# Optimization experiments

Measured on AMD Instinct MI355X. Metric: run time of the kernel, lower is better.

The kernel has to match this reference:

```python
import jax, jax.numpy as jnp
import numpy as np


def setup_inputs() -> dict:
    key = jax.random.key(0)
    ks = jax.random.split(key, 8)
    C = 256
    Cq = C // 8  # 32
    B, H, W = 4, 64, 64
    x = jax.random.normal(ks[0], (B, C, H, W), dtype=jnp.float32)
    wq = jax.random.normal(ks[1], (Cq, C), dtype=jnp.float32) * (1.0 / np.sqrt(C))
    bq = jax.random.normal(ks[2], (Cq,), dtype=jnp.float32) * 0.01
    wk = jax.random.normal(ks[3], (Cq, C), dtype=jnp.float32) * (1.0 / np.sqrt(C))
    bk = jax.random.normal(ks[4], (Cq,), dtype=jnp.float32) * 0.01
    wv = jax.random.normal(ks[5], (C, C), dtype=jnp.float32) * (1.0 / np.sqrt(C))
    bv = jax.random.normal(ks[6], (C,), dtype=jnp.float32) * 0.01
    gamma = jax.random.normal(ks[7], (1,), dtype=jnp.float32)
    return {"x": x, "wq": wq, "bq": bq, "wk": wk, "bk": bk,
            "wv": wv, "bv": bv, "gamma": gamma}


def reference(x, wq, bq, wk, bk, wv, bv, gamma):
    B, C, H, W = x.shape
    N = H * W
    xf = x.reshape(B, C, N)  # [B, C, N] flattened spatial
    # 1x1 convs == per-position linear projections
    q = jnp.einsum('oc,bcn->bno', wq, xf) + bq          # [B, N, Cq]
    k = jnp.einsum('oc,bcn->bon', wk, xf) + bk[:, None]  # [B, Cq, N]
    v = jnp.einsum('oc,bcn->bon', wv, xf) + bv[:, None]  # [B, C, N]
    attn = jax.nn.softmax(jnp.einsum('bnc,bcm->bnm', q, k), axis=-1)  # [B, N, N]
    # out[b,c,n] = sum_m v[b,c,m] * attn[n,m]
    out = jnp.einsum('bcm,bnm->bcn', v, attn).reshape(B, C, H, W)
    return gamma[0] * out + x
```

## Files before the change

kernel.cpp:

```cpp
#include <hip/hip_runtime.h>

#define BB 4
#define CC 256
#define CQ 32
#define NN 4096

#define QT_OFF 0
#define KT_OFF (BB*NN*CQ)
#define VT_OFF (2*BB*NN*CQ)
#define WB_OFF (VT_OFF + BB*CC*NN)
#define BIAS_OFF (WB_OFF + 320*256)

#define LDS_BARRIER() asm volatile("s_waitcnt lgkmcnt(0)\ns_barrier" ::: "memory")

typedef __attribute__((ext_vector_type(8))) short bf16x8;
typedef __attribute__((ext_vector_type(4))) short bf16x4;
typedef __attribute__((ext_vector_type(4))) float f32x4;

__device__ inline unsigned short f2bf(float f) {
    unsigned int u = __float_as_uint(f);
    u += 0x7fffu + ((u >> 16) & 1u);
    return (unsigned short)(u >> 16);
}

__global__ __launch_bounds__(256) void prepw_kernel(
    const float* __restrict__ wq, const float* __restrict__ bq,
    const float* __restrict__ wk, const float* __restrict__ bk,
    const float* __restrict__ wv, const float* __restrict__ bv,
    unsigned short* __restrict__ ws)
{
    unsigned short* Wb = ws + WB_OFF;
    float* Bias = (float*)(ws + BIAS_OFF);
    int idx = blockIdx.x * 256 + threadIdx.x;
    if (idx < 320 * 256) {
        int row = idx >> 8, col = idx & 255;
        float v = row < 32 ? wq[row * 256 + col]
                : row < 64 ? wk[(row - 32) * 256 + col]
                           : wv[(row - 64) * 256 + col];
        Wb[idx] = f2bf(v);
    }
    if (idx < 320)
        Bias[idx] = idx < 32 ? bq[idx] : idx < 64 ? bk[idx - 32] : bv[idx - 64];
}

__global__ __launch_bounds__(256, 2) void qkv_kernel(
    const float* __restrict__ x, unsigned short* __restrict__ ws)
{
    __shared__ __align__(16) unsigned short xs[32][264];
    __shared__ __align__(16) unsigned short vs[256][40];
    const int t = threadIdx.x;
    const int w = t >> 6, l = t & 63, quad = l >> 4, lc = l & 15;
    const int b = blockIdx.y, n0 = blockIdx.x * 32;

    unsigned short* qT = ws + QT_OFF;
    unsigned short* kT = ws + KT_OFF;
    const unsigned short* Wb = ws + WB_OFF;
    const float* Bias = (const float*)(ws + BIAS_OFF);

    const float* xb = x + (size_t)(b * CC) * NN + n0;
    {
        const int nq = t & 7, swz = (nq & 3) << 3;
#pragma unroll
        for (int u = 0; u < 2; ++u) {
            const int c0 = (t >> 3) * 4 + u * 128;
            f32x4 r0 = *(const f32x4*)&xb[(size_t)(c0 + 0) * NN + nq * 4];
            f32x4 r1 = *(const f32x4*)&xb[(size_t)(c0 + 1) * NN + nq * 4];
            f32x4 r2 = *(const f32x4*)&xb[(size_t)(c0 + 2) * NN + nq * 4];
            f32x4 r3 = *(const f32x4*)&xb[(size_t)(c0 + 3) * NN + nq * 4];
            const int cs = c0 ^ swz;
#pragma unroll
            for (int k = 0; k < 4; ++k) {
                bf16x4 w4;
                w4[0] = (short)f2bf(r0[k]);
                w4[1] = (short)f2bf(r1[k]);
                w4[2] = (short)f2bf(r2[k]);
                w4[3] = (short)f2bf(r3[k]);
                *(bf16x4*)&xs[nq * 4 + k][cs] = w4;
            }
        }
    }
    __syncthreads();

    f32x4 acc[5][2];
#pragma unroll
    for (int j = 0; j < 5; ++j) {
        f32x4 b4 = *(const f32x4*)&Bias[(w * 5 + j) * 16 + quad * 4];
        acc[j][0] = b4; acc[j][1] = b4;
    }

#pragma unroll
    for (int s = 0; s < 8; ++s) {
        bf16x8 Af[5], Bf[2];
#pragma unroll
        for (int j = 0; j < 5; ++j)
            Af[j] = *(const bf16x8*)&Wb[((w * 5 + j) * 16 + lc) * 256 + s * 32 + quad * 8];
#pragma unroll
        for (int nt = 0; nt < 2; ++nt) {
            int pos = nt * 16 + lc;
            int col = (s * 32 + quad * 8) ^ (((pos >> 2) & 3) << 3);
            Bf[nt] = *(const bf16x8*)&xs[pos][col];
        }
#pragma unroll
        for (int j = 0; j < 5; ++j)
#pragma unroll
            for (int nt = 0; nt < 2; ++nt)
                acc[j][nt] = __builtin_amdgcn_mfma_f32_16x16x32_bf16(Af[j], Bf[nt], acc[j][nt], 0, 0, 0);
    }

#pragma unroll
    for (int j = 0; j < 5; ++j) {
        int ot = w * 5 + j;
#pragma unroll
        for (int nt = 0; nt < 2; ++nt) {
            if (ot < 4) {
                bf16x4 pk;
#pragma unroll
                for (int i = 0; i < 4; ++i) pk[i] = (short)f2bf(acc[j][nt][i]);
                unsigned short* bas = (ot < 2 ? qT : kT);
                int ocl = (ot & 1) * 16 + quad * 4;
                *(bf16x4*)&bas[((size_t)(b * NN + n0 + nt * 16 + lc)) * CQ + ocl] = pk;
            } else {
#pragma unroll
                for (int i = 0; i < 4; ++i)
                    vs[(ot - 4) * 16 + quad * 4 + i][nt * 16 + lc] = f2bf(acc[j][nt][i]);
            }
        }
    }
    __syncthreads();

    const int mt = n0 >> 6, hb = (n0 >> 5) & 1;
    unsigned short* vt = ws + VT_OFF + ((size_t)(b * 64 + mt) * 16) * 1024 + hb * 512;
#pragma unroll
    for (int p = 0; p < 4; ++p) {
        int ci = p * 256 + t;
        int ct = ci >> 6, g = (ci >> 4) & 3, lcp = ci & 15;
        bf16x8 chunk = *(const bf16x8*)&vs[ct * 16 + lcp][g * 8];
        *(bf16x8*)&vt[(size_t)ct * 1024 + g * 128 + lcp * 8] = chunk;
    }
}

__global__ __launch_bounds__(512, 2) void attn_kernel(
    const float* __restrict__ x, const unsigned short* __restrict__ ws,
    const float* __restrict__ gamma, float* __restrict__ out)
{
    __shared__ __align__(16) unsigned short Ps[2][4][4][512];
    __shared__ __align__(16) float lSpart[2][64];

    const int t = threadIdx.x;
    const int w = t >> 6, l = t & 63, quad = l >> 4, lc = l & 15;
    const int id = blockIdx.x, xcd = id & 7;
    const int b = xcd >> 1;
    const int n0 = (((id >> 3) << 1) | (xcd & 1)) * 64;

    const int qg = w & 3;
    const int kh = w >> 2;
    const int cb = w * 32;

    const unsigned short* qT = ws + QT_OFF;
    const unsigned short* kb = ws + KT_OFF + (size_t)b * NN * CQ;
    const unsigned short* vb = ws + VT_OFF + ((size_t)b << 20);

    const bf16x8 bqf =
        *(const bf16x8*)&qT[((size_t)(b * NN + n0 + qg * 16 + lc)) * CQ + quad * 8];

    bf16x8 kA[4], kB[4];
    auto loadK = [&](bf16x8* kr, int tt) {
        int m0 = (tt & 31) * 128 + kh * 64;
#pragma unroll
        for (int j = 0; j < 4; ++j)
            kr[j] = *(const bf16x8*)&kb[(size_t)(m0 + j * 16 + lc) * CQ + quad * 8];
    };

    bf16x8 vA[2][4], vB[2][4];
    auto loadV = [&](bf16x8 (*vr)[4], int tt) {
#pragma unroll
        for (int c = 0; c < 2; ++c) {
            int ct = w * 2 + c;
#pragma unroll
            for (int k4 = 0; k4 < 4; ++k4) {
                int m = (tt & 31) * 2 + (k4 >> 1);
                vr[c][k4] = *(const bf16x8*)&vb[((size_t)m * 16 + ct) * 1024 + (k4 & 1) * 512 + l * 8];
            }
        }
    };

    f32x4 acc[4][2];
#pragma unroll
    for (int i = 0; i < 4; ++i)
#pragma unroll
        for (int j = 0; j < 2; ++j) acc[i][j] = (f32x4){0.f, 0.f, 0.f, 0.f};
    f32x4 sn[4];
    float lacc = 0.f;
    const f32x4 z = {0.f, 0.f, 0.f, 0.f};

    auto expj = [&](int pp, int j) {
        bf16x4 pk;
#pragma unroll
        for (int i = 0; i < 4; ++i) {
            float p = __expf(sn[j][i]);
            lacc += p;
            pk[i] = (short)f2bf(p);
        }
        int ks = kh * 2 + (j >> 1);
        int lanep = ((2 * j + (quad >> 1)) & 3) * 16 + lc;
        *(bf16x4*)&Ps[pp][qg][ks][lanep * 8 + (quad & 1) * 4] = pk;
    };

    auto pvks = [&](int ks, bf16x8 (*vr)[4], const bf16x8* ap) {
        __builtin_amdgcn_s_setprio(1);
#pragma unroll
        for (int qs = 0; qs < 4; ++qs)
#pragma unroll
            for (int c = 0; c < 2; ++c)
                acc[qs][c] = __builtin_amdgcn_mfma_f32_16x16x32_bf16(ap[qs], vr[c][ks], acc[qs][c], 0, 0, 0);
        __builtin_amdgcn_s_setprio(0);
    };

    auto body = [&](int tt, int pp, bf16x8* kUse, bf16x8* kNext,
                    bf16x8 (*vUse)[4], bf16x8 (*vNext)[4]) {
        loadV(vNext, tt + 1);
#pragma unroll
        for (int j = 0; j < 4; ++j)
            sn[j] = __builtin_amdgcn_mfma_f32_16x16x32_bf16(kUse[j], bqf, z, 0, 0, 0);
        loadK(kNext, tt + 2);
#pragma unroll
        for (int ks = 0; ks < 4; ++ks) {
            bf16x8 ap[4];
#pragma unroll
            for (int qs = 0; qs < 4; ++qs)
                ap[qs] = *(const bf16x8*)&Ps[pp][qs][ks][l * 8];
            expj(pp ^ 1, ks);
            pvks(ks, vUse, ap);
        }
        LDS_BARRIER();
    };

    loadK(kA, 0);
#pragma unroll
    for (int j = 0; j < 4; ++j)
        sn[j] = __builtin_amdgcn_mfma_f32_16x16x32_bf16(kA[j], bqf, z, 0, 0, 0);
    loadK(kA, 1);
#pragma unroll
    for (int j = 0; j < 4; ++j) expj(0, j);
    loadV(vA, 0);
    LDS_BARRIER();

    for (int it = 0; it < 15; ++it) {
        body(2 * it,     0, kA, kB, vA, vB);
        body(2 * it + 1, 1, kB, kA, vB, vA);
    }
    body(30, 0, kA, kB, vA, vB);
#pragma unroll
    for (int ks = 0; ks < 4; ++ks) {
        bf16x8 ap[4];
#pragma unroll
        for (int qs = 0; qs < 4; ++qs)
            ap[qs] = *(const bf16x8*)&Ps[1][qs][ks][l * 8];
        pvks(ks, vB, ap);
    }

    lacc += __shfl_xor(lacc, 16);
    lacc += __shfl_xor(lacc, 32);
    if (quad == 0) lSpart[kh][qg * 16 + lc] = lacc;
    LDS_BARRIER();

    const float g = gamma[0];
#pragma unroll
    for (int qs = 0; qs < 4; ++qs) {
        f32x4 l0 = *(const f32x4*)&lSpart[0][qs * 16 + quad * 4];
        f32x4 l1 = *(const f32x4*)&lSpart[1][qs * 16 + quad * 4];
        f32x4 rl;
#pragma unroll
        for (int i = 0; i < 4; ++i) rl[i] = 1.f / (l0[i] + l1[i]);
#pragma unroll
        for (int c2 = 0; c2 < 2; ++c2) {
            int c = cb + c2 * 16 + lc;
            size_t base = ((size_t)(b * CC + c)) * NN + n0 + qs * 16 + quad * 4;
            f32x4 xr = *(const f32x4*)&x[base];
            f32x4 o;
#pragma unroll
            for (int i = 0; i < 4; ++i) o[i] = g * acc[qs][c2][i] * rl[i] + xr[i];
            *(f32x4*)&out[base] = o;
        }
    }
}

extern "C" void kernel_launch(void* const* d_in, const int* in_sizes, int n_in,
                              void* d_out, int out_size, void* d_ws, size_t ws_size,
                              hipStream_t stream) {
    const float* x     = (const float*)d_in[0];
    const float* wq    = (const float*)d_in[1];
    const float* bq    = (const float*)d_in[2];
    const float* wk    = (const float*)d_in[3];
    const float* bk    = (const float*)d_in[4];
    const float* wv    = (const float*)d_in[5];
    const float* bv    = (const float*)d_in[6];
    const float* gamma = (const float*)d_in[7];
    float* out = (float*)d_out;
    unsigned short* ws = (unsigned short*)d_ws;

    prepw_kernel<<<320, 256, 0, stream>>>(wq, bq, wk, bk, wv, bv, ws);
    dim3 g1(NN / 32, BB);
    qkv_kernel<<<g1, 256, 0, stream>>>(x, ws);
    attn_kernel<<<256, 512, 0, stream>>>(x, ws, gamma, out);
}
```

Measured before the change: 145.0 us.

## Specialize warps into QK/softmax producers and PV consumers

```diff
diff --git a/kernel.cpp b/kernel.cpp
--- a/kernel.cpp
+++ b/kernel.cpp
@@ -144,143 +144,157 @@
     const float* __restrict__ gamma, float* __restrict__ out)
 {
     __shared__ __align__(16) unsigned short Ps[2][4][4][512];
-    __shared__ __align__(16) float lSpart[2][64];
+    __shared__ __align__(16) float lS[64];
 
     const int t = threadIdx.x;
     const int w = t >> 6, l = t & 63, quad = l >> 4, lc = l & 15;
     const int id = blockIdx.x, xcd = id & 7;
     const int b = xcd >> 1;
     const int n0 = (((id >> 3) << 1) | (xcd & 1)) * 64;
-
-    const int qg = w & 3;
-    const int kh = w >> 2;
-    const int cb = w * 32;
+    const int r = w >> 1;
 
     const unsigned short* qT = ws + QT_OFF;
     const unsigned short* kb = ws + KT_OFF + (size_t)b * NN * CQ;
     const unsigned short* vb = ws + VT_OFF + ((size_t)b << 20);
 
-    const bf16x8 bqf =
-        *(const bf16x8*)&qT[((size_t)(b * NN + n0 + qg * 16 + lc)) * CQ + quad * 8];
-
-    bf16x8 kA[4], kB[4];
-    auto loadK = [&](bf16x8* kr, int tt) {
-        int m0 = (tt & 31) * 128 + kh * 64;
-#pragma unroll
-        for (int j = 0; j < 4; ++j)
-            kr[j] = *(const bf16x8*)&kb[(size_t)(m0 + j * 16 + lc) * CQ + quad * 8];
-    };
-
-    bf16x8 vA[2][4], vB[2][4];
-    auto loadV = [&](bf16x8 (*vr)[4], int tt) {
-#pragma unroll
-        for (int c = 0; c < 2; ++c) {
-            int ct = w * 2 + c;
-#pragma unroll
-            for (int k4 = 0; k4 < 4; ++k4) {
-                int m = (tt & 31) * 2 + (k4 >> 1);
-                vr[c][k4] = *(const bf16x8*)&vb[((size_t)m * 16 + ct) * 1024 + (k4 & 1) * 512 + l * 8];
-            }
-        }
-    };
-
-    f32x4 acc[4][2];
-#pragma unroll
-    for (int i = 0; i < 4; ++i)
-#pragma unroll
-        for (int j = 0; j < 2; ++j) acc[i][j] = (f32x4){0.f, 0.f, 0.f, 0.f};
-    f32x4 sn[4];
-    float lacc = 0.f;
-    const f32x4 z = {0.f, 0.f, 0.f, 0.f};
-
-    auto expj = [&](int pp, int j) {
-        bf16x4 pk;
-#pragma unroll
-        for (int i = 0; i < 4; ++i) {
-            float p = __expf(sn[j][i]);
-            lacc += p;
-            pk[i] = (short)f2bf(p);
-        }
-        int ks = kh * 2 + (j >> 1);
-        int lanep = ((2 * j + (quad >> 1)) & 3) * 16 + lc;
-        *(bf16x4*)&Ps[pp][qg][ks][lanep * 8 + (quad & 1) * 4] = pk;
-    };
-
-    auto pvks = [&](int ks, bf16x8 (*vr)[4], const bf16x8* ap) {
-        __builtin_amdgcn_s_setprio(1);
-#pragma unroll
-        for (int qs = 0; qs < 4; ++qs)
-#pragma unroll
-            for (int c = 0; c < 2; ++c)
-                acc[qs][c] = __builtin_amdgcn_mfma_f32_16x16x32_bf16(ap[qs], vr[c][ks], acc[qs][c], 0, 0, 0);
-        __builtin_amdgcn_s_setprio(0);
-    };
-
-    auto body = [&](int tt, int pp, bf16x8* kUse, bf16x8* kNext,
-                    bf16x8 (*vUse)[4], bf16x8 (*vNext)[4]) {
-        loadV(vNext, tt + 1);
-#pragma unroll
-        for (int j = 0; j < 4; ++j)
-            sn[j] = __builtin_amdgcn_mfma_f32_16x16x32_bf16(kUse[j], bqf, z, 0, 0, 0);
-        loadK(kNext, tt + 2);
-#pragma unroll
-        for (int ks = 0; ks < 4; ++ks) {
+    if ((w & 1) == 0) {
+        const int qg = r;
+        const bf16x8 bqf =
+            *(const bf16x8*)&qT[((size_t)(b * NN + n0 + qg * 16 + lc)) * CQ + quad * 8];
+        const f32x4 z = {0.f, 0.f, 0.f, 0.f};
+
+        bf16x8 kA[8], kB[8];
+        auto loadK = [&](bf16x8* kr, int tt) {
+            int m0 = (tt & 31) * 128;
+#pragma unroll
+            for (int j = 0; j < 8; ++j)
+                kr[j] = *(const bf16x8*)&kb[(size_t)(m0 + j * 16 + lc) * CQ + quad * 8];
+        };
+
+        f32x4 sn[8];
+        float lacc = 0.f;
+
+        auto expj = [&](int pp, int j) {
+            bf16x4 pk;
+#pragma unroll
+            for (int i = 0; i < 4; ++i) {
+                float p = __expf(sn[j][i]);
+                lacc += p;
+                pk[i] = (short)f2bf(p);
+            }
+            int ks = j >> 1;
+            int lanep = ((2 * j + (quad >> 1)) & 3) * 16 + lc;
+            *(bf16x4*)&Ps[pp][qg][ks][lanep * 8 + (quad & 1) * 4] = pk;
+        };
+
+        auto qkbody = [&](int tt, bf16x8* kUse, bf16x8* kNext) {
+#pragma unroll
+            for (int j = 0; j < 8; ++j)
+                sn[j] = __builtin_amdgcn_mfma_f32_16x16x32_bf16(kUse[j], bqf, z, 0, 0, 0);
+            loadK(kNext, tt + 2);
+#pragma unroll
+            for (int j = 0; j < 8; ++j) expj((tt + 1) & 1, j);
+            LDS_BARRIER();
+        };
+
+        loadK(kA, 0);
+#pragma unroll
+        for (int j = 0; j < 8; ++j)
+            sn[j] = __builtin_amdgcn_mfma_f32_16x16x32_bf16(kA[j], bqf, z, 0, 0, 0);
+        loadK(kA, 1);
+#pragma unroll
+        for (int j = 0; j < 8; ++j) expj(0, j);
+        LDS_BARRIER();
+
+        for (int it = 0; it < 15; ++it) {
+            qkbody(2 * it,     kA, kB);
+            qkbody(2 * it + 1, kB, kA);
+        }
+        qkbody(30, kA, kB);
+
+        lacc += __shfl_xor(lacc, 16);
+        lacc += __shfl_xor(lacc, 32);
+        if (quad == 0) lS[qg * 16 + lc] = lacc;
+        LDS_BARRIER();
+    } else {
+        const int cq4 = r;
+
+        f32x4 acc[4][4];
+#pragma unroll
+        for (int i = 0; i < 4; ++i)
+#pragma unroll
+            for (int j = 0; j < 4; ++j) acc[i][j] = (f32x4){0.f, 0.f, 0.f, 0.f};
+
+        bf16x8 vcur[4], vnxt[4];
+        auto loadVks = [&](bf16x8* vr, int tt, int ks) {
+            int m = (tt & 31) * 2 + (ks >> 1);
+#pragma unroll
+            for (int c = 0; c < 4; ++c) {
+                int ct = cq4 * 4 + c;
+                vr[c] = *(const bf16x8*)&vb[((size_t)m * 16 + ct) * 1024 + (ks & 1) * 512 + l * 8];
+            }
+        };
+
+        auto pvstep = [&](int pp, int ks, const bf16x8* vr) {
             bf16x8 ap[4];
 #pragma unroll
             for (int qs = 0; qs < 4; ++qs)
                 ap[qs] = *(const bf16x8*)&Ps[pp][qs][ks][l * 8];
-            expj(pp ^ 1, ks);
-            pvks(ks, vUse, ap);
-        }
+            __builtin_amdgcn_s_setprio(1);
+#pragma unroll
+            for (int qs = 0; qs < 4; ++qs)
+#pragma unroll
+                for (int c = 0; c < 4; ++c)
+                    acc[qs][c] = __builtin_amdgcn_mfma_f32_16x16x32_bf16(ap[qs], vr[c], acc[qs][c], 0, 0, 0);
+            __builtin_amdgcn_s_setprio(0);
+        };
+
+        loadVks(vcur, 0, 0);
         LDS_BARRIER();
-    };
-
-    loadK(kA, 0);
-#pragma unroll
-    for (int j = 0; j < 4; ++j)
-        sn[j] = __builtin_amdgcn_mfma_f32_16x16x32_bf16(kA[j], bqf, z, 0, 0, 0);
-    loadK(kA, 1);
-#pragma unroll
-    for (int j = 0; j < 4; ++j) expj(0, j);
-    loadV(vA, 0);
-    LDS_BARRIER();
-
-    for (int it = 0; it < 15; ++it) {
-        body(2 * it,     0, kA, kB, vA, vB);
-        body(2 * it + 1, 1, kB, kA, vB, vA);
-    }
-    body(30, 0, kA, kB, vA, vB);
-#pragma unroll
-    for (int ks = 0; ks < 4; ++ks) {
-        bf16x8 ap[4];
-#pragma unroll
-        for (int qs = 0; qs < 4; ++qs)
-            ap[qs] = *(const bf16x8*)&Ps[1][qs][ks][l * 8];
-        pvks(ks, vB, ap);
-    }
-
-    lacc += __shfl_xor(lacc, 16);
-    lacc += __shfl_xor(lacc, 32);
-    if (quad == 0) lSpart[kh][qg * 16 + lc] = lacc;
-    LDS_BARRIER();
-
-    const float g = gamma[0];
-#pragma unroll
-    for (int qs = 0; qs < 4; ++qs) {
-        f32x4 l0 = *(const f32x4*)&lSpart[0][qs * 16 + quad * 4];
-        f32x4 l1 = *(const f32x4*)&lSpart[1][qs * 16 + quad * 4];
-        f32x4 rl;
-#pragma unroll
-        for (int i = 0; i < 4; ++i) rl[i] = 1.f / (l0[i] + l1[i]);
-#pragma unroll
-        for (int c2 = 0; c2 < 2; ++c2) {
-            int c = cb + c2 * 16 + lc;
-            size_t base = ((size_t)(b * CC + c)) * NN + n0 + qs * 16 + quad * 4;
-            f32x4 xr = *(const f32x4*)&x[base];
-            f32x4 o;
-#pragma unroll
-            for (int i = 0; i < 4; ++i) o[i] = g * acc[qs][c2][i] * rl[i] + xr[i];
-            *(f32x4*)&out[base] = o;
+
+        for (int tt = 0; tt < 31; ++tt) {
+            int pp = tt & 1;
+#pragma unroll
+            for (int ks = 0; ks < 4; ++ks) {
+                if (ks & 1) {
+                    loadVks(vcur, ks == 3 ? tt + 1 : tt, (ks + 1) & 3);
+                    pvstep(pp, ks, vnxt);
+                } else {
+                    loadVks(vnxt, tt, ks + 1);
+                    pvstep(pp, ks, vcur);
+                }
+            }
+            LDS_BARRIER();
+        }
+#pragma unroll
+        for (int ks = 0; ks < 4; ++ks) {
+            if (ks & 1) {
+                if (ks < 3) loadVks(vcur, 31, ks + 1);
+                pvstep(1, ks, vnxt);
+            } else {
+                loadVks(vnxt, 31, ks + 1);
+                pvstep(1, ks, vcur);
+            }
+        }
+        LDS_BARRIER();
+
+        const float g = gamma[0];
+#pragma unroll
+        for (int qs = 0; qs < 4; ++qs) {
+            f32x4 lv = *(const f32x4*)&lS[qs * 16 + quad * 4];
+            f32x4 rl;
+#pragma unroll
+            for (int i = 0; i < 4; ++i) rl[i] = 1.f / lv[i];
+#pragma unroll
+            for (int c2 = 0; c2 < 4; ++c2) {
+                int c = cq4 * 64 + c2 * 16 + lc;
+                size_t base = ((size_t)(b * CC + c)) * NN + n0 + qs * 16 + quad * 4;
+                f32x4 xr = *(const f32x4*)&x[base];
+                f32x4 o;
+#pragma unroll
+                for (int i = 0; i < 4; ++i) o[i] = g * acc[qs][c2][i] * rl[i] + xr[i];
+                *(f32x4*)&out[base] = o;
+            }
         }
     }
 }
```

Measured after the change: 151.5 us. 1.04x slower.

## Warp-specialize attention kernel into QK/softmax producer and PV consumer waves

Applied to the files above, without the earlier changes.

```diff
diff --git a/kernel.cpp b/kernel.cpp
--- a/kernel.cpp
+++ b/kernel.cpp
@@ -139,7 +139,7 @@
     }
 }
 
-__global__ __launch_bounds__(512, 2) void attn_kernel(
+__global__ __launch_bounds__(1024, 4) void attn_kernel(
     const float* __restrict__ x, const unsigned short* __restrict__ ws,
     const float* __restrict__ gamma, float* __restrict__ out)
 {
@@ -151,136 +151,145 @@
     const int id = blockIdx.x, xcd = id & 7;
     const int b = xcd >> 1;
     const int n0 = (((id >> 3) << 1) | (xcd & 1)) * 64;
-
-    const int qg = w & 3;
-    const int kh = w >> 2;
-    const int cb = w * 32;
+    const int role = (w + (w >> 2)) & 1;
+    const int r = (w >> 2) * 2 + ((w & 3) >> 1);
 
     const unsigned short* qT = ws + QT_OFF;
     const unsigned short* kb = ws + KT_OFF + (size_t)b * NN * CQ;
-    const unsigned short* vb = ws + VT_OFF + ((size_t)b << 20);
-
-    const bf16x8 bqf =
-        *(const bf16x8*)&qT[((size_t)(b * NN + n0 + qg * 16 + lc)) * CQ + quad * 8];
-
-    bf16x8 kA[4], kB[4];
-    auto loadK = [&](bf16x8* kr, int tt) {
-        int m0 = (tt & 31) * 128 + kh * 64;
+    const unsigned short* vbase = ws + VT_OFF + ((size_t)b << 20);
+
+    if (role == 0) {
+        const int qg = r & 3, kh = r >> 2;
+        const bf16x8 bqf =
+            *(const bf16x8*)&qT[((size_t)(b * NN + n0 + qg * 16 + lc)) * CQ + quad * 8];
+        const f32x4 z = {0.f, 0.f, 0.f, 0.f};
+
+        bf16x8 kA[4], kB[4];
+        auto loadK = [&](bf16x8* kr, int tt) {
+            int m0 = (tt & 31) * 128 + kh * 64;
+#pragma unroll
+            for (int j = 0; j < 4; ++j)
+                kr[j] = *(const bf16x8*)&kb[(size_t)(m0 + j * 16 + lc) * CQ + quad * 8];
+        };
+
+        f32x4 sn[4];
+        float lacc = 0.f;
+
+        auto expj = [&](int pp, int j) {
+            bf16x4 pk;
+#pragma unroll
+            for (int i = 0; i < 4; ++i) {
+                float p = __expf(sn[j][i]);
+                lacc += p;
+                pk[i] = (short)f2bf(p);
+            }
+            int ks = kh * 2 + (j >> 1);
+            int lanep = ((2 * j + (quad >> 1)) & 3) * 16 + lc;
+            *(bf16x4*)&Ps[pp][qg][ks][lanep * 8 + (quad & 1) * 4] = pk;
+        };
+
+        auto qkbody = [&](int tt, bf16x8* kUse, bf16x8* kNext) {
+#pragma unroll
+            for (int j = 0; j < 4; ++j)
+                sn[j] = __builtin_amdgcn_mfma_f32_16x16x32_bf16(kUse[j], bqf, z, 0, 0, 0);
+            loadK(kNext, tt + 2);
+#pragma unroll
+            for (int j = 0; j < 4; ++j) expj((tt + 1) & 1, j);
+            LDS_BARRIER();
+        };
+
+        loadK(kA, 0);
 #pragma unroll
         for (int j = 0; j < 4; ++j)
-            kr[j] = *(const bf16x8*)&kb[(size_t)(m0 + j * 16 + lc) * CQ + quad * 8];
-    };
-
-    bf16x8 vA[2][4], vB[2][4];
-    auto loadV = [&](bf16x8 (*vr)[4], int tt) {
-#pragma unroll
-        for (int c = 0; c < 2; ++c) {
-            int ct = w * 2 + c;
-#pragma unroll
-            for (int k4 = 0; k4 < 4; ++k4) {
-                int m = (tt & 31) * 2 + (k4 >> 1);
-                vr[c][k4] = *(const bf16x8*)&vb[((size_t)m * 16 + ct) * 1024 + (k4 & 1) * 512 + l * 8];
-            }
-        }
-    };
-
-    f32x4 acc[4][2];
-#pragma unroll
-    for (int i = 0; i < 4; ++i)
-#pragma unroll
-        for (int j = 0; j < 2; ++j) acc[i][j] = (f32x4){0.f, 0.f, 0.f, 0.f};
-    f32x4 sn[4];
-    float lacc = 0.f;
-    const f32x4 z = {0.f, 0.f, 0.f, 0.f};
-
-    auto expj = [&](int pp, int j) {
-        bf16x4 pk;
-#pragma unroll
-        for (int i = 0; i < 4; ++i) {
-            float p = __expf(sn[j][i]);
-            lacc += p;
-            pk[i] = (short)f2bf(p);
-        }
-        int ks = kh * 2 + (j >> 1);
-        int lanep = ((2 * j + (quad >> 1)) & 3) * 16 + lc;
-        *(bf16x4*)&Ps[pp][qg][ks][lanep * 8 + (quad & 1) * 4] = pk;
-    };
-
-    auto pvks = [&](int ks, bf16x8 (*vr)[4], const bf16x8* ap) {
-        __builtin_amdgcn_s_setprio(1);
-#pragma unroll
-        for (int qs = 0; qs < 4; ++qs)
-#pragma unroll
-            for (int c = 0; c < 2; ++c)
-                acc[qs][c] = __builtin_amdgcn_mfma_f32_16x16x32_bf16(ap[qs], vr[c][ks], acc[qs][c], 0, 0, 0);
-        __builtin_amdgcn_s_setprio(0);
-    };
-
-    auto body = [&](int tt, int pp, bf16x8* kUse, bf16x8* kNext,
-                    bf16x8 (*vUse)[4], bf16x8 (*vNext)[4]) {
-        loadV(vNext, tt + 1);
-#pragma unroll
-        for (int j = 0; j < 4; ++j)
-            sn[j] = __builtin_amdgcn_mfma_f32_16x16x32_bf16(kUse[j], bqf, z, 0, 0, 0);
-        loadK(kNext, tt + 2);
-#pragma unroll
-        for (int ks = 0; ks < 4; ++ks) {
+            sn[j] = __builtin_amdgcn_mfma_f32_16x16x32_bf16(kA[j], bqf, z, 0, 0, 0);
+        loadK(kA, 1);
+#pragma unroll
+        for (int j = 0; j < 4; ++j) expj(0, j);
+        LDS_BARRIER();
+
+        for (int it = 0; it < 15; ++it) {
+            qkbody(2 * it,     kA, kB);
+            qkbody(2 * it + 1, kB, kA);
+        }
+        qkbody(30, kA, kB);
+
+        lacc += __shfl_xor(lacc, 16);
+        lacc += __shfl_xor(lacc, 32);
+        if (quad == 0) lSpart[kh][qg * 16 + lc] = lacc;
+        LDS_BARRIER();
+    } else {
+        const int rv = r;
+
+        f32x4 acc[4][2];
+#pragma unroll
+        for (int i = 0; i < 4; ++i)
+#pragma unroll
+            for (int j = 0; j < 2; ++j) acc[i][j] = (f32x4){0.f, 0.f, 0.f, 0.f};
+
+        bf16x8 va[2][2], vb2[2][2];
+        auto loadVhalf = [&](bf16x8 (*vr)[2], int tt, int half) {
+            int m = (tt & 31) * 2 + half;
+#pragma unroll
+            for (int c = 0; c < 2; ++c) {
+                int ct = rv * 2 + c;
+#pragma unroll
+                for (int kk = 0; kk < 2; ++kk)
+                    vr[c][kk] = *(const bf16x8*)&vbase[((size_t)m * 16 + ct) * 1024 + kk * 512 + l * 8];
+            }
+        };
+
+        auto pvks = [&](int pp, int ks, const bf16x8& v0, const bf16x8& v1) {
             bf16x8 ap[4];
 #pragma unroll
             for (int qs = 0; qs < 4; ++qs)
                 ap[qs] = *(const bf16x8*)&Ps[pp][qs][ks][l * 8];
-            expj(pp ^ 1, ks);
-            pvks(ks, vUse, ap);
-        }
+            __builtin_amdgcn_s_setprio(1);
+#pragma unroll
+            for (int qs = 0; qs < 4; ++qs) {
+                acc[qs][0] = __builtin_amdgcn_mfma_f32_16x16x32_bf16(ap[qs], v0, acc[qs][0], 0, 0, 0);
+                acc[qs][1] = __builtin_amdgcn_mfma_f32_16x16x32_bf16(ap[qs], v1, acc[qs][1], 0, 0, 0);
+            }
+            __builtin_amdgcn_s_setprio(0);
+        };
+
+        loadVhalf(va, 0, 0);
+        loadVhalf(vb2, 0, 1);
         LDS_BARRIER();
-    };
-
-    loadK(kA, 0);
-#pragma unroll
-    for (int j = 0; j < 4; ++j)
-        sn[j] = __builtin_amdgcn_mfma_f32_16x16x32_bf16(kA[j], bqf, z, 0, 0, 0);
-    loadK(kA, 1);
-#pragma unroll
-    for (int j = 0; j < 4; ++j) expj(0, j);
-    loadV(vA, 0);
-    LDS_BARRIER();
-
-    for (int it = 0; it < 15; ++it) {
-        body(2 * it,     0, kA, kB, vA, vB);
-        body(2 * it + 1, 1, kB, kA, vB, vA);
-    }
-    body(30, 0, kA, kB, vA, vB);
-#pragma unroll
-    for (int ks = 0; ks < 4; ++ks) {
-        bf16x8 ap[4];
-#pragma unroll
-        for (int qs = 0; qs < 4; ++qs)
-            ap[qs] = *(const bf16x8*)&Ps[1][qs][ks][l * 8];
-        pvks(ks, vB, ap);
-    }
-
-    lacc += __shfl_xor(lacc, 16);
-    lacc += __shfl_xor(lacc, 32);
-    if (quad == 0) lSpart[kh][qg * 16 + lc] = lacc;
-    LDS_BARRIER();
-
-    const float g = gamma[0];
-#pragma unroll
-    for (int qs = 0; qs < 4; ++qs) {
-        f32x4 l0 = *(const f32x4*)&lSpart[0][qs * 16 + quad * 4];
-        f32x4 l1 = *(const f32x4*)&lSpart[1][qs * 16 + quad * 4];
-        f32x4 rl;
-#pragma unroll
-        for (int i = 0; i < 4; ++i) rl[i] = 1.f / (l0[i] + l1[i]);
-#pragma unroll
-        for (int c2 = 0; c2 < 2; ++c2) {
-            int c = cb + c2 * 16 + lc;
-            size_t base = ((size_t)(b * CC + c)) * NN + n0 + qs * 16 + quad * 4;
-            f32x4 xr = *(const f32x4*)&x[base];
-            f32x4 o;
-#pragma unroll
-            for (int i = 0; i < 4; ++i) o[i] = g * acc[qs][c2][i] * rl[i] + xr[i];
-            *(f32x4*)&out[base] = o;
+
+        for (int tt = 0; tt < 31; ++tt) {
+            int pp = tt & 1;
+            pvks(pp, 0, va[0][0], va[1][0]);
+            pvks(pp, 1, va[0][1], va[1][1]);
+            loadVhalf(va, tt + 1, 0);
+            pvks(pp, 2, vb2[0][0], vb2[1][0]);
+            pvks(pp, 3, vb2[0][1], vb2[1][1]);
+            loadVhalf(vb2, tt + 1, 1);
+            LDS_BARRIER();
+        }
+        pvks(1, 0, va[0][0], va[1][0]);
+        pvks(1, 1, va[0][1], va[1][1]);
+        pvks(1, 2, vb2[0][0], vb2[1][0]);
+        pvks(1, 3, vb2[0][1], vb2[1][1]);
+        LDS_BARRIER();
+
+        const float g = gamma[0];
+#pragma unroll
+        for (int qs = 0; qs < 4; ++qs) {
+            f32x4 l0 = *(const f32x4*)&lSpart[0][qs * 16 + quad * 4];
+            f32x4 l1 = *(const f32x4*)&lSpart[1][qs * 16 + quad * 4];
+            f32x4 rl;
+#pragma unroll
+            for (int i = 0; i < 4; ++i) rl[i] = 1.f / (l0[i] + l1[i]);
+#pragma unroll
+            for (int c2 = 0; c2 < 2; ++c2) {
+                int c = rv * 32 + c2 * 16 + lc;
+                size_t base = ((size_t)(b * CC + c)) * NN + n0 + qs * 16 + quad * 4;
+                f32x4 xr = *(const f32x4*)&x[base];
+                f32x4 o;
+#pragma unroll
+                for (int i = 0; i < 4; ++i) o[i] = g * acc[qs][c2][i] * rl[i] + xr[i];
+                *(f32x4*)&out[base] = o;
+            }
         }
     }
 }
@@ -302,5 +311,5 @@
     prepw_kernel<<<320, 256, 0, stream>>>(wq, bq, wk, bk, wv, bv, ws);
     dim3 g1(NN / 32, BB);
     qkv_kernel<<<g1, 256, 0, stream>>>(x, ws);
-    attn_kernel<<<256, 512, 0, stream>>>(x, ws, gamma, out);
-}
+    attn_kernel<<<256, 1024, 0, stream>>>(x, ws, gamma, out);
+}
```

Result: faster. 136.7 us (-5.7%).
